# Kernel optimization log

Measured on AMD Instinct MI355X. Metric: run time of the kernel, lower is better.

Reference implementation:

```python
import jax, jax.numpy as jnp
import numpy as np

N = 100000      # nodes
E = 1600000     # edges (avg degree 16)
IN = 128        # in_channels
OUT = 32        # out_channels -> hidden = 2*OUT = 64


def gcn_conv(x, src, dst, W, b):
    """PyG GCNConv: linear transform, add self loops, symmetric D^-1/2 (A+I) D^-1/2 aggregation."""
    n = x.shape[0]
    h = x @ W                                   # [N, out]
    # degree with self loops (all edge weights = 1)
    deg = jax.ops.segment_sum(jnp.ones(src.shape[0], h.dtype), dst, num_segments=n) + 1.0
    dinv = jax.lax.rsqrt(deg)                   # [N]
    norm = dinv[src] * dinv[dst]                # [E]
    agg = jax.ops.segment_sum(h[src] * norm[:, None], dst, num_segments=n)
    agg = agg + h * (dinv * dinv)[:, None]      # self-loop contribution
    return agg + b


def setup_inputs() -> dict:
    key = jax.random.key(0)
    ks = jax.random.split(key, 8)
    x = jax.random.normal(ks[0], (N, IN), jnp.float32)
    edge_index = jax.random.randint(ks[1], (2, E), 0, N, jnp.int32)
    H = 2 * OUT
    W1 = jax.random.normal(ks[2], (IN, H), jnp.float32) / jnp.sqrt(jnp.float32(IN))
    b1 = jnp.zeros((H,), jnp.float32)
    W_mu = jax.random.normal(ks[3], (H, OUT), jnp.float32) / jnp.sqrt(jnp.float32(H))
    b_mu = jnp.zeros((OUT,), jnp.float32)
    W_logstd = jax.random.normal(ks[4], (H, OUT), jnp.float32) / jnp.sqrt(jnp.float32(H))
    b_logstd = jnp.zeros((OUT,), jnp.float32)
    return {"x": x, "edge_index": edge_index, "W1": W1, "b1": b1,
            "W_mu": W_mu, "b_mu": b_mu, "W_logstd": W_logstd, "b_logstd": b_logstd}


def reference(x, edge_index, W1, b1, W_mu, b_mu, W_logstd, b_logstd):
    src, dst = edge_index[0], edge_index[1]
    h = jax.nn.relu(gcn_conv(x, src, dst, W1, b1))          # [N, 2*OUT]
    mu = gcn_conv(h, src, dst, W_mu, b_mu)                  # [N, OUT]
    logstd = gcn_conv(h, src, dst, W_logstd, b_logstd)      # [N, OUT]
    return mu, logstd
```

## Files before the change

kernel.cpp:

```cpp
#include <hip/hip_runtime.h>
#include <hip/hip_fp16.h>

#define IN_C 128
#define H 64
#define NBITS 9
#define BSZ 512
#define CAP 16384
#define BINCHUNK 4096

typedef unsigned int u32;
typedef __attribute__((ext_vector_type(8))) _Float16 h8;
typedef __attribute__((ext_vector_type(4))) float f4;

__device__ __forceinline__ int excl_scan256(int v, int* wsum, int tid) {
    int lane = tid & 63, wid = tid >> 6;
    int s = v;
    #pragma unroll
    for (int off = 1; off < 64; off <<= 1) {
        int t = __shfl_up(s, off);
        if (lane >= off) s += t;
    }
    if (lane == 63) wsum[wid] = s;
    __syncthreads();
    if (tid == 0) {
        int c = 0;
        #pragma unroll
        for (int i = 0; i < 4; ++i) { int t = wsum[i]; wsum[i] = c; c += t; }
    }
    __syncthreads();
    return s - v + wsum[wid];
}

__device__ __forceinline__ int excl_scan512(int v, int* wsum, int tid) {
    int lane = tid & 63, wid = tid >> 6;
    int s = v;
    #pragma unroll
    for (int off = 1; off < 64; off <<= 1) {
        int t = __shfl_up(s, off);
        if (lane >= off) s += t;
    }
    if (lane == 63) wsum[wid] = s;
    __syncthreads();
    if (tid == 0) {
        int c = 0;
        #pragma unroll
        for (int i = 0; i < 8; ++i) { int t = wsum[i]; wsum[i] = c; c += t; }
    }
    __syncthreads();
    return s - v + wsum[wid];
}

__global__ __launch_bounds__(256) void k_init(int* __restrict__ bucketFill,
                                              __half* __restrict__ z0,
                                              __half* __restrict__ z1,
                                              const float* __restrict__ W1,
                                              const float* __restrict__ Wmu,
                                              const float* __restrict__ Wls,
                                              _Float16* __restrict__ W1T,
                                              _Float16* __restrict__ WT2) {
    int tid = threadIdx.x;
    int gt = blockIdx.x * 256 + tid;
    if (blockIdx.x == 0) {
        bucketFill[tid] = 0;
        if (tid < H) { z0[tid] = __float2half(0.f); z1[tid] = __float2half(0.f); }
    }
    for (int t = gt; t < 64 * 128; t += gridDim.x * 256) {
        int col = t >> 7, k = t & 127;
        W1T[t] = (_Float16)W1[k * 64 + col];
    }
    for (int t = gt; t < 64 * 64; t += gridDim.x * 256) {
        int col = t >> 6, k = t & 63;
        WT2[t] = (_Float16)((col < 32) ? Wmu[k * 32 + col] : Wls[k * 32 + (col - 32)]);
    }
}

__device__ __forceinline__ void mm1_tile_mfma(int tile, int t256, int n,
                                              const float* __restrict__ x,
                                              const _Float16* __restrict__ W1T,
                                              __half* __restrict__ out) {
    int wave = t256 >> 6, lane = t256 & 63;
    int cl = lane & 15;
    int kg = lane >> 4;
    int arow = tile * 64 + wave * 16 + cl;
    int na = min(arow, n - 1);
    const float4* x4 = (const float4*)x;
    float4 xr[8];
    #pragma unroll
    for (int kb = 0; kb < 4; ++kb) {
        int k0 = kb * 32 + kg * 8;
        xr[2 * kb]     = x4[(size_t)na * 32 + (k0 >> 2)];
        xr[2 * kb + 1] = x4[(size_t)na * 32 + (k0 >> 2) + 1];
    }
    f4 zero4 = {0.f, 0.f, 0.f, 0.f};
    f4 acc[4] = {zero4, zero4, zero4, zero4};
    #pragma unroll
    for (int kb = 0; kb < 4; ++kb) {
        int k0 = kb * 32 + kg * 8;
        float4 va = xr[2 * kb];
        float4 vb = xr[2 * kb + 1];
        h8 a;
        a[0] = (_Float16)va.x; a[1] = (_Float16)va.y; a[2] = (_Float16)va.z; a[3] = (_Float16)va.w;
        a[4] = (_Float16)vb.x; a[5] = (_Float16)vb.y; a[6] = (_Float16)vb.z; a[7] = (_Float16)vb.w;
        #pragma unroll
        for (int c = 0; c < 4; ++c) {
            h8 b = *(const h8*)&W1T[((c * 16 + cl) << 7) + k0];
            acc[c] = __builtin_amdgcn_mfma_f32_16x16x32_f16(a, b, acc[c], 0, 0, 0);
        }
    }
    int rbase = tile * 64 + wave * 16 + kg * 4;
    #pragma unroll
    for (int r = 0; r < 4; ++r) {
        int orow = rbase + r;
        if (orow < n) {
            #pragma unroll
            for (int c = 0; c < 4; ++c)
                out[(size_t)orow * 64 + c * 16 + cl] = __float2half((float)acc[c][r]);
        }
    }
}

struct SMemBin {
    u32 staged[BINCHUNK]; unsigned char stagedB[BINCHUNK];
    int lhist[256], lbase[256], gbase[256], lfill[256]; int wsum[4];
};

__global__ __launch_bounds__(256) void k_binmm(const int* __restrict__ src,
                                               const int* __restrict__ dst,
                                               int E, int n, int nbin,
                                               int* __restrict__ bucketFill,
                                               u32* __restrict__ binned,
                                               const float* __restrict__ x,
                                               const _Float16* __restrict__ W1T,
                                               __half* __restrict__ Ah) {
    __shared__ SMemBin sm;
    int bid = blockIdx.x, tid = threadIdx.x;
    if (bid < nbin) {
        int kbeg = bid * BINCHUNK;
        int cnt = min(BINCHUNK, E - kbeg);
        sm.lhist[tid] = 0; sm.lfill[tid] = 0;
        __syncthreads();
        for (int t = tid; t < cnt; t += 256)
            atomicAdd(&sm.lhist[dst[kbeg + t] >> NBITS], 1);
        __syncthreads();
        int v = sm.lhist[tid];
        int ex = excl_scan256(v, sm.wsum, tid);
        sm.lbase[tid] = ex;
        sm.gbase[tid] = v ? atomicAdd(&bucketFill[tid], v) : 0;
        __syncthreads();
        for (int t = tid; t < cnt; t += 256) {
            int d = dst[kbeg + t];
            int s = src[kbeg + t];
            int bk = d >> NBITS;
            int p = sm.lbase[bk] + atomicAdd(&sm.lfill[bk], 1);
            sm.staged[p] = ((u32)(d & (BSZ - 1)) << 23) | (u32)s;
            sm.stagedB[p] = (unsigned char)bk;
        }
        __syncthreads();
        for (int t = tid; t < cnt; t += 256) {
            int bk = sm.stagedB[t];
            binned[(size_t)bk * CAP + sm.gbase[bk] + (t - sm.lbase[bk])] = sm.staged[t];
        }
    } else {
        mm1_tile_mfma(bid - nbin, tid, n, x, W1T, Ah);
    }
}

__global__ __launch_bounds__(512) void k_bucket(const u32* __restrict__ binned,
                                                const int* __restrict__ bucketFill,
                                                u32* __restrict__ rowdesc,
                                                float* __restrict__ dinvp,
                                                int* __restrict__ colidx,
                                                __half* __restrict__ Ah, int n) {
    __shared__ int cnt[BSZ];
    __shared__ int loff[BSZ];
    __shared__ float sdinv[BSZ];
    __shared__ int wsum[8];
    int b = blockIdx.x, tid = threadIdx.x;
    int ebeg = b * CAP;
    int fill = bucketFill[b];
    cnt[tid] = 0;
    __syncthreads();
    for (int e = tid; e < fill; e += 512)
        atomicAdd(&cnt[binned[ebeg + e] >> 23], 1);
    __syncthreads();
    int c0 = cnt[tid];
    int ex = excl_scan512(c0, wsum, tid);
    loff[tid] = ex;
    int node0 = (b << NBITS) + tid;
    float d0 = rsqrtf((float)c0 + 1.0f);
    sdinv[tid] = d0;
    if (node0 < n) {
        rowdesc[node0] = ((u32)(ebeg + ex) << 10) | (u32)min(c0, 1023);
        dinvp[node0] = d0;
    }
    __syncthreads();
    cnt[tid] = 0;
    __syncthreads();
    for (int e = tid; e < fill; e += 512) {
        u32 pv = binned[ebeg + e];
        int ln = pv >> 23;
        int pos = ebeg + loff[ln] + atomicAdd(&cnt[ln], 1);
        colidx[pos] = (int)(pv & 0x7FFFFF);
    }
    int nvalid = min(n - (b << NBITS), BSZ);
    uint4* rows = (uint4*)(Ah + ((size_t)b << NBITS) * 64);
    union U { uint4 u; __half2 h[4]; };
    for (int t = tid; t < nvalid * 8; t += 512) {
        float d = sdinv[t >> 3];
        U v; v.u = rows[t];
        #pragma unroll
        for (int q = 0; q < 4; ++q) {
            float2 f = __half22float2(v.h[q]);
            v.h[q] = __floats2half2_rn(f.x * d, f.y * d);
        }
        rows[t] = v.u;
    }
}

template <bool L1, typename OutT>
__global__ __launch_bounds__(256) void k_gather(const __half* __restrict__ hs,
                                                OutT* __restrict__ out,
                                                const u32* __restrict__ rowdesc,
                                                const int* __restrict__ colidx,
                                                const float* __restrict__ dinv,
                                                const float* __restrict__ bias, int n) {
    int wid = threadIdx.x >> 6, lane = threadIdx.x & 63;
    int nbase = blockIdx.x * 8 + wid * 2;
    if (nbase >= n) return;
    int es = lane >> 3;
    int cc = lane & 7;
    const uint4* hs16 = (const uint4*)hs;
    union U { uint4 u; __half2 h[4]; };

    u32 rdv[2]; float div_[2]; U selfv[2]; int civ[2];
    #pragma unroll
    for (int i = 0; i < 2; ++i) {
        int node = min(nbase + i, n - 1);
        rdv[i] = rowdesc[node];
        div_[i] = dinv[node];
        selfv[i].u = hs16[((u32)node << 3) | cc];
    }
    #pragma unroll
    for (int i = 0; i < 2; ++i) {
        int beg = (int)(rdv[i] >> 10), deg = (int)(rdv[i] & 1023);
        civ[i] = (lane < deg) ? colidx[beg + lane] : n;
    }
    U r0[2][2];
    #pragma unroll
    for (int i = 0; i < 2; ++i) {
        #pragma unroll
        for (int j = 0; j < 2; ++j) {
            int s = __shfl(civ[i], 8 * j + es);
            r0[i][j].u = hs16[((u32)s << 3) | cc];
        }
    }
    U r1[2][2];
    #pragma unroll
    for (int i = 0; i < 2; ++i) {
        int deg = (int)(rdv[i] & 1023);
        if (deg > 16) {
            #pragma unroll
            for (int j = 0; j < 2; ++j) {
                int s = __shfl(civ[i], 8 * (j + 2) + es);
                r1[i][j].u = hs16[((u32)s << 3) | cc];
            }
        }
    }

    #pragma unroll
    for (int i = 0; i < 2; ++i) {
        int node = nbase + i;
        if (node >= n) break;
        int beg = (int)(rdv[i] >> 10);
        int deg = (int)(rdv[i] & 1023);
        int end = beg + deg;
        float a[8] = {0.f, 0.f, 0.f, 0.f, 0.f, 0.f, 0.f, 0.f};
        #pragma unroll
        for (int j = 0; j < 2; ++j) {
            #pragma unroll
            for (int q = 0; q < 4; ++q) {
                float2 f = __half22float2(r0[i][j].h[q]);
                a[2 * q] += f.x; a[2 * q + 1] += f.y;
            }
        }
        if (deg > 16) {
            #pragma unroll
            for (int j = 0; j < 2; ++j)
                #pragma unroll
                for (int q = 0; q < 4; ++q) {
                    float2 f = __half22float2(r1[i][j].h[q]);
                    a[2 * q] += f.x; a[2 * q + 1] += f.y;
                }
        }
        if (deg > 32) {
            U r[4];
            #pragma unroll
            for (int j = 0; j < 4; ++j) {
                int s = __shfl(civ[i], (8 * (j + 4) + es) & 63);
                r[j].u = hs16[((u32)s << 3) | cc];
            }
            #pragma unroll
            for (int j = 0; j < 4; ++j)
                #pragma unroll
                for (int q = 0; q < 4; ++q) {
                    float2 f = __half22float2(r[j].h[q]);
                    a[2 * q] += f.x; a[2 * q + 1] += f.y;
                }
        }
        for (int e = beg + 64 + es; e < end; e += 8) {
            int s = colidx[e];
            U r; r.u = hs16[((u32)s << 3) | cc];
            #pragma unroll
            for (int q = 0; q < 4; ++q) {
                float2 f = __half22float2(r.h[q]);
                a[2 * q] += f.x; a[2 * q + 1] += f.y;
            }
        }
        #pragma unroll
        for (int q = 0; q < 8; ++q) {
            a[q] += __shfl_xor(a[q], 8);
            a[q] += __shfl_xor(a[q], 16);
            a[q] += __shfl_xor(a[q], 32);
        }

        if (lane < 8) {
            float di = div_[i];
            #pragma unroll
            for (int q = 0; q < 4; ++q) {
                float2 f = __half22float2(selfv[i].h[q]);
                a[2 * q] += f.x; a[2 * q + 1] += f.y;
            }
            float v[8];
            #pragma unroll
            for (int q = 0; q < 8; ++q) v[q] = di * a[q];
            if (L1) {
                float4 b0 = ((const float4*)bias)[2 * cc];
                float4 b1 = ((const float4*)bias)[2 * cc + 1];
                v[0] = fmaxf(v[0] + b0.x, 0.f) * di;
                v[1] = fmaxf(v[1] + b0.y, 0.f) * di;
                v[2] = fmaxf(v[2] + b0.z, 0.f) * di;
                v[3] = fmaxf(v[3] + b0.w, 0.f) * di;
                v[4] = fmaxf(v[4] + b1.x, 0.f) * di;
                v[5] = fmaxf(v[5] + b1.y, 0.f) * di;
                v[6] = fmaxf(v[6] + b1.z, 0.f) * di;
                v[7] = fmaxf(v[7] + b1.w, 0.f) * di;
            }
            if constexpr (sizeof(OutT) == 2) {
                U o;
                o.h[0] = __floats2half2_rn(v[0], v[1]);
                o.h[1] = __floats2half2_rn(v[2], v[3]);
                o.h[2] = __floats2half2_rn(v[4], v[5]);
                o.h[3] = __floats2half2_rn(v[6], v[7]);
                ((uint4*)out)[((u32)node << 3) | cc] = o.u;
            } else {
                ((float4*)out)[((u32)node << 4) | (2 * cc)]     = make_float4(v[0], v[1], v[2], v[3]);
                ((float4*)out)[((u32)node << 4) | (2 * cc + 1)] = make_float4(v[4], v[5], v[6], v[7]);
            }
        }
    }
}

__global__ __launch_bounds__(256) void k_mm2(const __half* __restrict__ G,
                                             const _Float16* __restrict__ WT2,
                                             const float* __restrict__ bmu,
                                             const float* __restrict__ bls,
                                             float* __restrict__ out, int n) {
    int tile = blockIdx.x;
    int wave = threadIdx.x >> 6, lane = threadIdx.x & 63;
    int cl = lane & 15, kg = lane >> 4;
    int arow = tile * 64 + wave * 16 + cl;
    int na = min(arow, n - 1);
    const _Float16* Gf = (const _Float16*)G;
    f4 zero4 = {0.f, 0.f, 0.f, 0.f};
    f4 acc[4] = {zero4, zero4, zero4, zero4};
    #pragma unroll
    for (int kb = 0; kb < 2; ++kb) {
        int k0 = kb * 32 + kg * 8;
        h8 a = *(const h8*)&Gf[((size_t)na << 6) + k0];
        #pragma unroll
        for (int c = 0; c < 4; ++c) {
            h8 b = *(const h8*)&WT2[((c * 16 + cl) << 6) + k0];
            acc[c] = __builtin_amdgcn_mfma_f32_16x16x32_f16(a, b, acc[c], 0, 0, 0);
        }
    }
    int rbase = tile * 64 + wave * 16 + kg * 4;
    #pragma unroll
    for (int c = 0; c < 4; ++c) {
        int col = c * 16 + cl;
        float bv = (col < 32) ? bmu[col] : bls[col - 32];
        float* obase = (col < 32) ? (out + col) : (out + (size_t)n * 32 + (col - 32));
        #pragma unroll
        for (int r = 0; r < 4; ++r) {
            int orow = rbase + r;
            if (orow < n) obase[(size_t)orow * 32] = (float)acc[c][r] + bv;
        }
    }
}


extern "C" void kernel_launch(void* const* d_in, const int* in_sizes, int n_in,
                              void* d_out, int out_size, void* d_ws, size_t ws_size,
                              hipStream_t stream) {
    const float* x   = (const float*)d_in[0];
    const int*   ei  = (const int*)d_in[1];
    const float* W1  = (const float*)d_in[2];
    const float* b1  = (const float*)d_in[3];
    const float* Wmu = (const float*)d_in[4];
    const float* bmu = (const float*)d_in[5];
    const float* Wls = (const float*)d_in[6];
    const float* bls = (const float*)d_in[7];
    float* out = (float*)d_out;

    int n = in_sizes[0] / IN_C;
    int E = in_sizes[1] / 2;
    const int* srcp = ei;
    const int* dstp = ei + E;
    int NBUK = (n + BSZ - 1) >> NBITS;
    int nbin = (E + BINCHUNK - 1) / BINCHUNK;
    int ntiles = (n + 63) / 64;

    char* p = (char*)d_ws;
    __half* Ah  = (__half*)p; p += (size_t)(n + 1) * H * sizeof(__half);
    __half* Bh  = (__half*)p; p += (size_t)(n + 1) * H * sizeof(__half);
    __half* G   = (__half*)p; p += (size_t)n * H * sizeof(__half);
    float* dinv = (float*)p;  p += (size_t)n * sizeof(float);
    u32* rowdesc = (u32*)p;   p += (size_t)n * sizeof(u32);
    int* colidx = (int*)p;    p += (size_t)NBUK * CAP * sizeof(int);
    u32* binned = (u32*)p;    p += (size_t)NBUK * CAP * sizeof(u32);
    int* bucketFill = (int*)p; p += 256 * sizeof(int);
    _Float16* W1T = (_Float16*)p; p += 64 * 128 * sizeof(_Float16);
    _Float16* WT2 = (_Float16*)p; p += 64 * 64 * sizeof(_Float16);

    k_init<<<16, 256, 0, stream>>>(bucketFill, Ah + (size_t)n * H, Bh + (size_t)n * H,
                                   W1, Wmu, Wls, W1T, WT2);
    k_binmm<<<nbin + ntiles, 256, 0, stream>>>(srcp, dstp, E, n, nbin,
                                               bucketFill, binned, x, W1T, Ah);
    k_bucket<<<NBUK, 512, 0, stream>>>(binned, bucketFill, rowdesc, dinv, colidx, Ah, n);

    k_gather<true, __half><<<(n + 7) / 8, 256, 0, stream>>>(Ah, Bh, rowdesc, colidx, dinv, b1, n);
    k_gather<false, __half><<<(n + 7) / 8, 256, 0, stream>>>(Bh, G, rowdesc, colidx, dinv, nullptr, n);
    k_mm2<<<(n + 63) / 64, 256, 0, stream>>>(G, WT2, bmu, bls, out, n);
}
```

Baseline: 232.2 us.

## Fuse second-layer gather with the output MFMA matmul via shared memory

Merges the second aggregation kernel and the final 64x64 matmul into one kernel. Each block gathers 64 nodes into an LDS tile and then runs the MFMA projection from LDS. This drops the G intermediate's global write and read and one launch. The cost is a serial per-wave loop over 8 node pairs and a grid with 8x fewer blocks, which may hurt latency hiding for the irregular gather.

Result: no change. 234.7 us (+1.1%).

```diff
diff --git a/kernel.cpp b/kernel.cpp
--- a/kernel.cpp
+++ b/kernel.cpp
@@ -217,13 +217,12 @@
     }
 }
 
-template <bool L1, typename OutT>
-__global__ __launch_bounds__(256) void k_gather(const __half* __restrict__ hs,
-                                                OutT* __restrict__ out,
-                                                const u32* __restrict__ rowdesc,
-                                                const int* __restrict__ colidx,
-                                                const float* __restrict__ dinv,
-                                                const float* __restrict__ bias, int n) {
+__global__ __launch_bounds__(256) void k_gather1(const __half* __restrict__ hs,
+                                                 __half* __restrict__ out,
+                                                 const u32* __restrict__ rowdesc,
+                                                 const int* __restrict__ colidx,
+                                                 const float* __restrict__ dinv,
+                                                 const float* __restrict__ bias, int n) {
     int wid = threadIdx.x >> 6, lane = threadIdx.x & 63;
     int nbase = blockIdx.x * 8 + wid * 2;
     if (nbase >= n) return;
@@ -330,60 +329,166 @@
                 float2 f = __half22float2(selfv[i].h[q]);
                 a[2 * q] += f.x; a[2 * q + 1] += f.y;
             }
+            float4 b0 = ((const float4*)bias)[2 * cc];
+            float4 b1 = ((const float4*)bias)[2 * cc + 1];
             float v[8];
-            #pragma unroll
-            for (int q = 0; q < 8; ++q) v[q] = di * a[q];
-            if (L1) {
-                float4 b0 = ((const float4*)bias)[2 * cc];
-                float4 b1 = ((const float4*)bias)[2 * cc + 1];
-                v[0] = fmaxf(v[0] + b0.x, 0.f) * di;
-                v[1] = fmaxf(v[1] + b0.y, 0.f) * di;
-                v[2] = fmaxf(v[2] + b0.z, 0.f) * di;
-                v[3] = fmaxf(v[3] + b0.w, 0.f) * di;
-                v[4] = fmaxf(v[4] + b1.x, 0.f) * di;
-                v[5] = fmaxf(v[5] + b1.y, 0.f) * di;
-                v[6] = fmaxf(v[6] + b1.z, 0.f) * di;
-                v[7] = fmaxf(v[7] + b1.w, 0.f) * di;
-            }
-            if constexpr (sizeof(OutT) == 2) {
+            v[0] = fmaxf(di * a[0] + b0.x, 0.f) * di;
+            v[1] = fmaxf(di * a[1] + b0.y, 0.f) * di;
+            v[2] = fmaxf(di * a[2] + b0.z, 0.f) * di;
+            v[3] = fmaxf(di * a[3] + b0.w, 0.f) * di;
+            v[4] = fmaxf(di * a[4] + b1.x, 0.f) * di;
+            v[5] = fmaxf(di * a[5] + b1.y, 0.f) * di;
+            v[6] = fmaxf(di * a[6] + b1.z, 0.f) * di;
+            v[7] = fmaxf(di * a[7] + b1.w, 0.f) * di;
+            U o;
+            o.h[0] = __floats2half2_rn(v[0], v[1]);
+            o.h[1] = __floats2half2_rn(v[2], v[3]);
+            o.h[2] = __floats2half2_rn(v[4], v[5]);
+            o.h[3] = __floats2half2_rn(v[6], v[7]);
+            ((uint4*)out)[((u32)node << 3) | cc] = o.u;
+        }
+    }
+}
+
+__global__ __launch_bounds__(256) void k_gmm2(const __half* __restrict__ hs,
+                                              const u32* __restrict__ rowdesc,
+                                              const int* __restrict__ colidx,
+                                              const float* __restrict__ dinv,
+                                              const _Float16* __restrict__ WT2,
+                                              const float* __restrict__ bmu,
+                                              const float* __restrict__ bls,
+                                              float* __restrict__ out, int n) {
+    __shared__ _Float16 sg[64][72];
+    int wid = threadIdx.x >> 6, lane = threadIdx.x & 63;
+    int tile = blockIdx.x;
+    int es = lane >> 3;
+    int cc = lane & 7;
+    const uint4* hs16 = (const uint4*)hs;
+    union U { uint4 u; __half2 h[4]; };
+
+    for (int it = 0; it < 8; ++it) {
+        int nbase = tile * 64 + wid * 16 + it * 2;
+        if (nbase >= n) continue;
+        u32 rdv[2]; float div_[2]; U selfv[2]; int civ[2];
+        #pragma unroll
+        for (int i = 0; i < 2; ++i) {
+            int node = min(nbase + i, n - 1);
+            rdv[i] = rowdesc[node];
+            div_[i] = dinv[node];
+            selfv[i].u = hs16[((u32)node << 3) | cc];
+        }
+        #pragma unroll
+        for (int i = 0; i < 2; ++i) {
+            int beg = (int)(rdv[i] >> 10), deg = (int)(rdv[i] & 1023);
+            civ[i] = (lane < deg) ? colidx[beg + lane] : n;
+        }
+        U r0[2][2];
+        #pragma unroll
+        for (int i = 0; i < 2; ++i) {
+            #pragma unroll
+            for (int j = 0; j < 2; ++j) {
+                int s = __shfl(civ[i], 8 * j + es);
+                r0[i][j].u = hs16[((u32)s << 3) | cc];
+            }
+        }
+        U r1[2][2];
+        #pragma unroll
+        for (int i = 0; i < 2; ++i) {
+            int deg = (int)(rdv[i] & 1023);
+            if (deg > 16) {
+                #pragma unroll
+                for (int j = 0; j < 2; ++j) {
+                    int s = __shfl(civ[i], 8 * (j + 2) + es);
+                    r1[i][j].u = hs16[((u32)s << 3) | cc];
+                }
+            }
+        }
+        #pragma unroll
+        for (int i = 0; i < 2; ++i) {
+            int node = nbase + i;
+            if (node >= n) break;
+            int beg = (int)(rdv[i] >> 10);
+            int deg = (int)(rdv[i] & 1023);
+            int end = beg + deg;
+            float a[8] = {0.f, 0.f, 0.f, 0.f, 0.f, 0.f, 0.f, 0.f};
+            #pragma unroll
+            for (int j = 0; j < 2; ++j) {
+                #pragma unroll
+                for (int q = 0; q < 4; ++q) {
+                    float2 f = __half22float2(r0[i][j].h[q]);
+                    a[2 * q] += f.x; a[2 * q + 1] += f.y;
+                }
+            }
+            if (deg > 16) {
+                #pragma unroll
+                for (int j = 0; j < 2; ++j)
+                    #pragma unroll
+                    for (int q = 0; q < 4; ++q) {
+                        float2 f = __half22float2(r1[i][j].h[q]);
+                        a[2 * q] += f.x; a[2 * q + 1] += f.y;
+                    }
+            }
+            if (deg > 32) {
+                U r[4];
+                #pragma unroll
+                for (int j = 0; j < 4; ++j) {
+                    int s = __shfl(civ[i], (8 * (j + 4) + es) & 63);
+                    r[j].u = hs16[((u32)s << 3) | cc];
+                }
+                #pragma unroll
+                for (int j = 0; j < 4; ++j)
+                    #pragma unroll
+                    for (int q = 0; q < 4; ++q) {
+                        float2 f = __half22float2(r[j].h[q]);
+                        a[2 * q] += f.x; a[2 * q + 1] += f.y;
+                    }
+            }
+            for (int e = beg + 64 + es; e < end; e += 8) {
+                int s = colidx[e];
+                U r; r.u = hs16[((u32)s << 3) | cc];
+                #pragma unroll
+                for (int q = 0; q < 4; ++q) {
+                    float2 f = __half22float2(r.h[q]);
+                    a[2 * q] += f.x; a[2 * q + 1] += f.y;
+                }
+            }
+            #pragma unroll
+            for (int q = 0; q < 8; ++q) {
+                a[q] += __shfl_xor(a[q], 8);
+                a[q] += __shfl_xor(a[q], 16);
+                a[q] += __shfl_xor(a[q], 32);
+            }
+            if (lane < 8) {
+                float di = div_[i];
+                #pragma unroll
+                for (int q = 0; q < 4; ++q) {
+                    float2 f = __half22float2(selfv[i].h[q]);
+                    a[2 * q] += f.x; a[2 * q + 1] += f.y;
+                }
                 U o;
-                o.h[0] = __floats2half2_rn(v[0], v[1]);
-                o.h[1] = __floats2half2_rn(v[2], v[3]);
-                o.h[2] = __floats2half2_rn(v[4], v[5]);
-                o.h[3] = __floats2half2_rn(v[6], v[7]);
-                ((uint4*)out)[((u32)node << 3) | cc] = o.u;
-            } else {
-                ((float4*)out)[((u32)node << 4) | (2 * cc)]     = make_float4(v[0], v[1], v[2], v[3]);
-                ((float4*)out)[((u32)node << 4) | (2 * cc + 1)] = make_float4(v[4], v[5], v[6], v[7]);
-            }
-        }
-    }
-}
-
-__global__ __launch_bounds__(256) void k_mm2(const __half* __restrict__ G,
-                                             const _Float16* __restrict__ WT2,
-                                             const float* __restrict__ bmu,
-                                             const float* __restrict__ bls,
-                                             float* __restrict__ out, int n) {
-    int tile = blockIdx.x;
-    int wave = threadIdx.x >> 6, lane = threadIdx.x & 63;
+                o.h[0] = __floats2half2_rn(di * a[0], di * a[1]);
+                o.h[1] = __floats2half2_rn(di * a[2], di * a[3]);
+                o.h[2] = __floats2half2_rn(di * a[4], di * a[5]);
+                o.h[3] = __floats2half2_rn(di * a[6], di * a[7]);
+                *(uint4*)&sg[wid * 16 + it * 2 + i][cc * 8] = o.u;
+            }
+        }
+    }
+
     int cl = lane & 15, kg = lane >> 4;
-    int arow = tile * 64 + wave * 16 + cl;
-    int na = min(arow, n - 1);
-    const _Float16* Gf = (const _Float16*)G;
     f4 zero4 = {0.f, 0.f, 0.f, 0.f};
     f4 acc[4] = {zero4, zero4, zero4, zero4};
     #pragma unroll
     for (int kb = 0; kb < 2; ++kb) {
         int k0 = kb * 32 + kg * 8;
-        h8 a = *(const h8*)&Gf[((size_t)na << 6) + k0];
+        h8 a = *(const h8*)&sg[wid * 16 + cl][k0];
         #pragma unroll
         for (int c = 0; c < 4; ++c) {
             h8 b = *(const h8*)&WT2[((c * 16 + cl) << 6) + k0];
             acc[c] = __builtin_amdgcn_mfma_f32_16x16x32_f16(a, b, acc[c], 0, 0, 0);
         }
     }
-    int rbase = tile * 64 + wave * 16 + kg * 4;
+    int rbase = tile * 64 + wid * 16 + kg * 4;
     #pragma unroll
     for (int c = 0; c < 4; ++c) {
         int col = c * 16 + cl;
@@ -422,7 +527,6 @@
     char* p = (char*)d_ws;
     __half* Ah  = (__half*)p; p += (size_t)(n + 1) * H * sizeof(__half);
     __half* Bh  = (__half*)p; p += (size_t)(n + 1) * H * sizeof(__half);
-    __half* G   = (__half*)p; p += (size_t)n * H * sizeof(__half);
     float* dinv = (float*)p;  p += (size_t)n * sizeof(float);
     u32* rowdesc = (u32*)p;   p += (size_t)n * sizeof(u32);
     int* colidx = (int*)p;    p += (size_t)NBUK * CAP * sizeof(int);
@@ -437,7 +541,6 @@
                                                bucketFill, binned, x, W1T, Ah);
     k_bucket<<<NBUK, 512, 0, stream>>>(binned, bucketFill, rowdesc, dinv, colidx, Ah, n);
 
-    k_gather<true, __half><<<(n + 7) / 8, 256, 0, stream>>>(Ah, Bh, rowdesc, colidx, dinv, b1, n);
-    k_gather<false, __half><<<(n + 7) / 8, 256, 0, stream>>>(Bh, G, rowdesc, colidx, dinv, nullptr, n);
-    k_mm2<<<(n + 63) / 64, 256, 0, stream>>>(G, WT2, bmu, bls, out, n);
-}
+    k_gather1<<<(n + 7) / 8, 256, 0, stream>>>(Ah, Bh, rowdesc, colidx, dinv, b1, n);
+    k_gmm2<<<ntiles, 256, 0, stream>>>(Bh, rowdesc, colidx, dinv, WT2, bmu, bls, out, n);
+}
```
